# Optimization experiments

Measured on AMD Instinct MI355X. Metric: run time of the kernel, lower is better.

The kernel has to match this reference:

```python
import jax, jax.numpy as jnp
import numpy as np

B, S, D, H, E, K = 4, 2048, 1024, 2048, 8, 2
MU, GAMMA, LN_EPS = 0.7, 1.0, 1e-5


def setup_inputs() -> dict:
    key = jax.random.key(0)
    ks = jax.random.split(key, 8)
    inv_d = 1.0 / np.sqrt(D)
    inv_h = 1.0 / np.sqrt(H)
    return {
        "x": jax.random.normal(ks[0], (B, S, D), dtype=jnp.float32),
        "momentum": jax.random.normal(ks[1], (B, S, D), dtype=jnp.float32),
        "Wg": jax.random.normal(ks[2], (D, E), dtype=jnp.float32) * inv_d,
        "bg": jnp.zeros((E,), dtype=jnp.float32),
        "W1": jax.random.normal(ks[3], (E, D, H), dtype=jnp.float32) * inv_d,
        "b1": jnp.zeros((E, H), dtype=jnp.float32),
        "W2": jax.random.normal(ks[4], (E, H, D), dtype=jnp.float32) * inv_h,
        "b2": jnp.zeros((E, D), dtype=jnp.float32),
        "ln_g": jnp.ones((D,), dtype=jnp.float32),
        "ln_b": jnp.zeros((D,), dtype=jnp.float32),
    }


def reference(x, momentum, Wg, bg, W1, b1, W2, b2, ln_g, ln_b):
    # --- TopKGate: linear router, softmax over top-k logits, zeros elsewhere ---
    logits = jnp.einsum("bsd,de->bse", x, Wg) + bg            # [B,S,E]
    top_v, top_i = jax.lax.top_k(logits, K)                    # [B,S,K]
    top_w = jax.nn.softmax(top_v, axis=-1)                     # [B,S,K]
    gates = jnp.sum(jax.nn.one_hot(top_i, E, dtype=x.dtype) * top_w[..., None], axis=-2)  # [B,S,E]

    # --- Dense all-expert FFN (faithful to the original per-expert loop) ---
    h = jax.nn.relu(jnp.einsum("bsd,edh->bseh", x, W1) + b1)   # [B,S,E,H]
    eo = jnp.einsum("bseh,ehd->bsed", h, W2) + b2              # [B,S,E,D]
    expert_outputs = jnp.einsum("bse,bsed->bsd", gates, eo)    # [B,S,D]

    # --- Momentum update + residual + LayerNorm ---
    new_momentum = -expert_outputs + MU * momentum
    out = x + GAMMA * new_momentum
    mean = jnp.mean(out, axis=-1, keepdims=True)
    var = jnp.mean(jnp.square(out - mean), axis=-1, keepdims=True)
    out = (out - mean) * jax.lax.rsqrt(var + LN_EPS) * ln_g + ln_b
    return out, new_momentum
```

## Files before the change

### kernel.cpp

```cpp
#include <hip/hip_runtime.h>

#define TT 8192
#define DD 1024
#define HHH 2048
#define EE 8
#define MUf 0.7f
#define GAMMAf 1.0f
#define LNEPS 1e-5f

typedef __bf16 bf16x8 __attribute__((ext_vector_type(8)));
typedef float floatx4 __attribute__((ext_vector_type(4)));

__device__ __forceinline__ unsigned short f2bf(float f) {
  unsigned u = __float_as_uint(f);
  u += 0x7FFFu + ((u >> 16) & 1u);
  return (unsigned short)(u >> 16);
}
__device__ __forceinline__ float bf2f(unsigned short u) {
  return __uint_as_float(((unsigned)u) << 16);
}
__device__ __forceinline__ void load_lds16(const void* g, void* l) {
  __builtin_amdgcn_global_load_lds(
      (__attribute__((address_space(1))) void*)g,
      (__attribute__((address_space(3))) void*)l,
      16, 0, 0);
}

__global__ __launch_bounds__(256) void cvt_router_kernel(
    const float* __restrict__ x, const float* __restrict__ Wg, const float* __restrict__ bg,
    unsigned short* __restrict__ xb,
    int* __restrict__ pair_e, float* __restrict__ pair_w) {
  int tid = threadIdx.x;
  size_t gi = (size_t)blockIdx.x * 2048 + (size_t)tid * 8;
  const float4* s = (const float4*)(x + gi);
  float4 a = s[0], b = s[1];
  unsigned r0 = f2bf(a.x) | ((unsigned)f2bf(a.y) << 16);
  unsigned r1 = f2bf(a.z) | ((unsigned)f2bf(a.w) << 16);
  unsigned r2 = f2bf(b.x) | ((unsigned)f2bf(b.y) << 16);
  unsigned r3 = f2bf(b.z) | ((unsigned)f2bf(b.w) << 16);
  ((uint4*)xb)[blockIdx.x * 256 + tid] = make_uint4(r0, r1, r2, r3);

  float xa[8] = {a.x, a.y, a.z, a.w, b.x, b.y, b.z, b.w};
  int d0 = (tid & 127) * 8;
  const float* wbase = Wg + (size_t)d0 * EE;
  float acc[EE];
#pragma unroll
  for (int e = 0; e < EE; ++e) acc[e] = 0.f;
#pragma unroll
  for (int i = 0; i < 8; ++i) {
    float4 w0 = *(const float4*)(wbase + i * EE);
    float4 w1 = *(const float4*)(wbase + i * EE + 4);
    acc[0] += xa[i] * w0.x; acc[1] += xa[i] * w0.y;
    acc[2] += xa[i] * w0.z; acc[3] += xa[i] * w0.w;
    acc[4] += xa[i] * w1.x; acc[5] += xa[i] * w1.y;
    acc[6] += xa[i] * w1.z; acc[7] += xa[i] * w1.w;
  }
#pragma unroll
  for (int e = 0; e < EE; ++e) {
#pragma unroll
    for (int off = 32; off > 0; off >>= 1) acc[e] += __shfl_xor(acc[e], off);
  }
  __shared__ float rs[4][EE];
  int wv = tid >> 6;
  if ((tid & 63) == 0) {
#pragma unroll
    for (int e = 0; e < EE; ++e) rs[wv][e] = acc[e];
  }
  __syncthreads();
  if ((tid & 127) == 0) {
    int half = tid >> 7;
    int t = blockIdx.x * 2 + half;
    float v[EE];
#pragma unroll
    for (int e = 0; e < EE; ++e) v[e] = rs[2 * half][e] + rs[2 * half + 1][e] + bg[e];
    int i0 = 0;
#pragma unroll
    for (int e = 1; e < EE; ++e) if (v[e] > v[i0]) i0 = e;
    int i1 = (i0 == 0) ? 1 : 0;
#pragma unroll
    for (int e = 0; e < EE; ++e) if (e != i0 && v[e] > v[i1]) i1 = e;
    float w1e = __expf(v[i1] - v[i0]);
    float inv = 1.f / (1.f + w1e);
    pair_e[2 * t] = i0;     pair_w[2 * t] = inv;
    pair_e[2 * t + 1] = i1; pair_w[2 * t + 1] = w1e * inv;
  }
}

__global__ __launch_bounds__(256) void count_kernel(const int* __restrict__ pair_e,
                                                    int* __restrict__ counts) {
  __shared__ int lh[EE];
  int tid = threadIdx.x;
  if (tid < EE) lh[tid] = 0;
  __syncthreads();
  int p = blockIdx.x * 256 + tid;
  atomicAdd(&lh[pair_e[p]], 1);
  __syncthreads();
  if (tid < EE) atomicAdd(&counts[tid], lh[tid]);
}

__global__ void prefix_kernel(const int* __restrict__ counts, int* __restrict__ offs,
                              int* __restrict__ cursor) {
  if (threadIdx.x == 0) {
    int s = 0;
    for (int e = 0; e < EE; ++e) { offs[e] = s; cursor[e] = s; s += counts[e]; }
    offs[EE] = s;
  }
}

__global__ __launch_bounds__(256) void scatter_kernel(const int* __restrict__ pair_e,
                                                      int* __restrict__ cursor,
                                                      int* __restrict__ pair_rows) {
  __shared__ int lh[EE];
  __shared__ int lb[EE];
  int tid = threadIdx.x;
  if (tid < EE) lh[tid] = 0;
  __syncthreads();
  int p = blockIdx.x * 256 + tid;
  int e = pair_e[p];
  int r = atomicAdd(&lh[e], 1);
  __syncthreads();
  if (tid < EE) lb[tid] = atomicAdd(&cursor[tid], lh[tid]);
  __syncthreads();
  pair_rows[lb[e] + r] = p;
}

__global__ __launch_bounds__(256) void transpose_cvt_kernel(const float* __restrict__ in,
                                                            unsigned short* __restrict__ out,
                                                            int R, int C) {
  __shared__ float tile[32][33];
  int e = blockIdx.z;
  const float* src = in + (size_t)e * R * C;
  unsigned short* dst = out + (size_t)e * R * C;
  int c0 = blockIdx.x * 32, r0 = blockIdx.y * 32;
  int tx = threadIdx.x, ty = threadIdx.y;
#pragma unroll
  for (int i = 0; i < 32; i += 8)
    tile[ty + i][tx] = src[(size_t)(r0 + ty + i) * C + (c0 + tx)];
  __syncthreads();
#pragma unroll
  for (int i = 0; i < 32; i += 8)
    dst[(size_t)(c0 + ty + i) * R + (r0 + tx)] = f2bf(tile[tx][ty + i]);
}

template <int MODE>
__global__ __launch_bounds__(256, 3) void moe_gemm_kernel(
    const unsigned short* __restrict__ Amat, const unsigned short* __restrict__ Bmat,
    const float* __restrict__ bias, const int* __restrict__ offsets,
    const int* __restrict__ pair_rows, const float* __restrict__ pair_w,
    unsigned short* __restrict__ Out, int Kd, int Nd, int nxlog) {
  int d = blockIdx.x;
  int e = d & 7;
  int lin = d >> 3;
  int mt = lin >> nxlog;
  int n0 = (lin & ((1 << nxlog) - 1)) << 7;
  int off = offsets[e];
  int cnt = offsets[e + 1] - off;
  if (mt * 128 >= cnt) return;
  int tid = threadIdx.x;
  int lane = tid & 63, wid = tid >> 6;

  __shared__ unsigned short As[3][128 * 32];
  __shared__ unsigned short Bs[3][128 * 32];

  const unsigned short* Bex = Bmat + (size_t)e * Nd * Kd;

  int csw = (((tid & 3) ^ ((tid >> 2) & 3)) * 8);
  const unsigned short* aptr[2];
  const unsigned short* bptr[2];
#pragma unroll
  for (int P = 0; P < 2; ++P) {
    int row = P * 64 + (tid >> 2);
    int sa = mt * 128 + row;
    if (sa >= cnt) sa = cnt - 1;
    int gr = (MODE == 0) ? (pair_rows[off + sa] >> 1) : (off + sa);
    aptr[P] = Amat + (size_t)gr * Kd + csw;
    bptr[P] = Bex + (size_t)(n0 + row) * Kd + csw;
  }

  int wm = (wid >> 1) * 64, wn = (wid & 1) * 64;
  int lr = lane & 15;
  int t4 = lane >> 4;
  int lka = ((t4 ^ (lr & 3)) * 8);

  floatx4 acc[4][4];
#pragma unroll
  for (int m = 0; m < 4; ++m)
#pragma unroll
    for (int n = 0; n < 4; ++n) acc[m][n] = (floatx4){0.f, 0.f, 0.f, 0.f};

  int NT = Kd >> 5;
#pragma unroll
  for (int P = 0; P < 2; ++P) {
    load_lds16(aptr[P], &As[0][P * 2048] + tid * 8);
    load_lds16(bptr[P], &Bs[0][P * 2048] + tid * 8);
  }
#pragma unroll
  for (int P = 0; P < 2; ++P) {
    load_lds16(aptr[P] + 32, &As[1][P * 2048] + tid * 8);
    load_lds16(bptr[P] + 32, &Bs[1][P * 2048] + tid * 8);
  }

  for (int kt = 0; kt < NT; ++kt) {
    int pf = kt + 2;
    if (pf < NT) {
      int ko = pf * 32;
      int pb = pf - (pf / 3) * 3;
#pragma unroll
      for (int P = 0; P < 2; ++P) {
        load_lds16(aptr[P] + ko, &As[pb][P * 2048] + tid * 8);
        load_lds16(bptr[P] + ko, &Bs[pb][P * 2048] + tid * 8);
      }
    }
    asm volatile("s_waitcnt vmcnt(8)" ::: "memory");
    __builtin_amdgcn_s_barrier();
    int b = kt - (kt / 3) * 3;
    bf16x8 af[4], bfr[4];
#pragma unroll
    for (int m = 0; m < 4; ++m)
      af[m] = *(const bf16x8*)(&As[b][(wm + m * 16 + lr) * 32 + lka]);
#pragma unroll
    for (int n = 0; n < 4; ++n)
      bfr[n] = *(const bf16x8*)(&Bs[b][(wn + n * 16 + lr) * 32 + lka]);
#pragma unroll
    for (int m = 0; m < 4; ++m)
#pragma unroll
      for (int n = 0; n < 4; ++n)
        acc[m][n] = __builtin_amdgcn_mfma_f32_16x16x32_bf16(af[m], bfr[n], acc[m][n], 0, 0, 0);
    __builtin_amdgcn_sched_barrier(0);
    __builtin_amdgcn_s_barrier();
  }

  int rem = cnt - mt * 128;
  if (rem > 128) rem = 128;
#pragma unroll
  for (int m = 0; m < 4; ++m) {
#pragma unroll
    for (int j = 0; j < 4; ++j) {
      int lrr = wm + m * 16 + ((lane >> 4) << 2) + j;
      if (lrr < rem) {
        int s = mt * 128 + lrr;
        size_t orow;
        float scale = 1.f;
        if (MODE == 0) {
          orow = (size_t)(off + s) * Nd;
        } else {
          int p = pair_rows[off + s];
          orow = (size_t)p * Nd;
          scale = pair_w[p];
        }
#pragma unroll
        for (int n = 0; n < 4; ++n) {
          int col = n0 + wn + n * 16 + lr;
          float v = acc[m][n][j] + bias[e * Nd + col];
          if (MODE == 0) v = fmaxf(v, 0.f);
          else v *= scale;
          Out[orow + col] = f2bf(v);
        }
      }
    }
  }
}

__global__ __launch_bounds__(256) void final_kernel(
    const float* __restrict__ x, const float* __restrict__ mom,
    const unsigned short* __restrict__ pairout, const float* __restrict__ ln_g,
    const float* __restrict__ ln_b, float* __restrict__ outp, float* __restrict__ nmp) {
  int t = blockIdx.x, tid = threadIdx.x;
  int d0 = tid * 4;
  size_t rowoff = (size_t)t * DD;
  const unsigned short* p0 = pairout + (size_t)(2 * t) * DD;
  const unsigned short* p1 = p0 + DD;
  float4 xv = *(const float4*)(x + rowoff + d0);
  float4 mv = *(const float4*)(mom + rowoff + d0);
  ushort4 u0 = *(const ushort4*)(p0 + d0);
  ushort4 u1 = *(const ushort4*)(p1 + d0);
  float eo[4] = {bf2f(u0.x) + bf2f(u1.x), bf2f(u0.y) + bf2f(u1.y),
                 bf2f(u0.z) + bf2f(u1.z), bf2f(u0.w) + bf2f(u1.w)};
  float xa[4] = {xv.x, xv.y, xv.z, xv.w};
  float ma[4] = {mv.x, mv.y, mv.z, mv.w};
  float o[4], nm[4];
  float s1 = 0.f, s2 = 0.f;
#pragma unroll
  for (int j = 0; j < 4; ++j) {
    nm[j] = MUf * ma[j] - eo[j];
    o[j] = xa[j] + GAMMAf * nm[j];
    s1 += o[j];
    s2 += o[j] * o[j];
  }
  *(float4*)(nmp + rowoff + d0) = make_float4(nm[0], nm[1], nm[2], nm[3]);
#pragma unroll
  for (int off = 32; off > 0; off >>= 1) {
    s1 += __shfl_xor(s1, off);
    s2 += __shfl_xor(s2, off);
  }
  __shared__ float rs[8];
  int wid = tid >> 6, lane = tid & 63;
  if (lane == 0) { rs[wid] = s1; rs[4 + wid] = s2; }
  __syncthreads();
  s1 = rs[0] + rs[1] + rs[2] + rs[3];
  s2 = rs[4] + rs[5] + rs[6] + rs[7];
  float mean = s1 * (1.f / DD);
  float var = s2 * (1.f / DD) - mean * mean;
  float rstd = rsqrtf(var + LNEPS);
  float4 g = *(const float4*)(ln_g + d0);
  float4 bb = *(const float4*)(ln_b + d0);
  float ga[4] = {g.x, g.y, g.z, g.w}, ba[4] = {bb.x, bb.y, bb.z, bb.w};
  float res[4];
#pragma unroll
  for (int j = 0; j < 4; ++j) res[j] = (o[j] - mean) * rstd * ga[j] + ba[j];
  *(float4*)(outp + rowoff + d0) = make_float4(res[0], res[1], res[2], res[3]);
}

extern "C" void kernel_launch(void* const* d_in, const int* in_sizes, int n_in,
                              void* d_out, int out_size, void* d_ws, size_t ws_size,
                              hipStream_t stream) {
  const float* x   = (const float*)d_in[0];
  const float* mom = (const float*)d_in[1];
  const float* Wg  = (const float*)d_in[2];
  const float* bg  = (const float*)d_in[3];
  const float* W1  = (const float*)d_in[4];
  const float* b1  = (const float*)d_in[5];
  const float* W2  = (const float*)d_in[6];
  const float* b2  = (const float*)d_in[7];
  const float* lng = (const float*)d_in[8];
  const float* lnb = (const float*)d_in[9];
  (void)in_sizes; (void)n_in; (void)out_size; (void)ws_size;
  float* outp = (float*)d_out;
  float* nmp  = outp + (size_t)TT * DD;

  char* base = (char*)d_ws;
  size_t off = 0;
  auto carve = [&](size_t bytes) {
    void* p = base + off;
    off += (bytes + 255) & ~(size_t)255;
    return p;
  };
  unsigned short* xb   = (unsigned short*)carve((size_t)TT * DD * 2);
  unsigned short* w1t  = (unsigned short*)carve((size_t)EE * HHH * DD * 2);
  unsigned short* w2t  = (unsigned short*)carve((size_t)EE * DD * HHH * 2);
  unsigned short* hbuf = (unsigned short*)carve((size_t)2 * TT * HHH * 2);
  unsigned short* pout = (unsigned short*)carve((size_t)2 * TT * DD * 2);
  int*   pair_e    = (int*)carve((size_t)2 * TT * 4);
  float* pair_w    = (float*)carve((size_t)2 * TT * 4);
  int*   pair_rows = (int*)carve((size_t)2 * TT * 4);
  int*   counts    = (int*)carve(256);
  int*   offs      = (int*)carve(256);
  int*   cursor    = (int*)carve(256);

  hipMemsetAsync(counts, 0, EE * sizeof(int), stream);
  cvt_router_kernel<<<TT / 2, 256, 0, stream>>>(x, Wg, bg, xb, pair_e, pair_w);
  count_kernel<<<(2 * TT) / 256, 256, 0, stream>>>(pair_e, counts);
  prefix_kernel<<<1, 64, 0, stream>>>(counts, offs, cursor);
  scatter_kernel<<<(2 * TT) / 256, 256, 0, stream>>>(pair_e, cursor, pair_rows);
  transpose_cvt_kernel<<<dim3(HHH / 32, DD / 32, EE), dim3(32, 8, 1), 0, stream>>>(W1, w1t, DD, HHH);
  transpose_cvt_kernel<<<dim3(DD / 32, HHH / 32, EE), dim3(32, 8, 1), 0, stream>>>(W2, w2t, HHH, DD);
  moe_gemm_kernel<0><<<EE * (HHH / 128) * 128, 256, 0, stream>>>(
      xb, w1t, b1, offs, pair_rows, pair_w, hbuf, DD, HHH, 4);
  moe_gemm_kernel<1><<<EE * (DD / 128) * 128, 256, 0, stream>>>(
      hbuf, w2t, b2, offs, pair_rows, pair_w, pout, HHH, DD, 3);
  final_kernel<<<TT, 256, 0, stream>>>(x, mom, pout, lng, lnb, outp, nmp);
}
```

Baseline: 323.0 us.

## Vectorize weight transpose with 64x64 tiles and use single barrier per GEMM k-step

```diff
diff --git a/kernel.cpp b/kernel.cpp
--- a/kernel.cpp
+++ b/kernel.cpp
@@ -127,19 +127,32 @@
 __global__ __launch_bounds__(256) void transpose_cvt_kernel(const float* __restrict__ in,
                                                             unsigned short* __restrict__ out,
                                                             int R, int C) {
-  __shared__ float tile[32][33];
+  __shared__ float tile[64][65];
   int e = blockIdx.z;
   const float* src = in + (size_t)e * R * C;
   unsigned short* dst = out + (size_t)e * R * C;
-  int c0 = blockIdx.x * 32, r0 = blockIdx.y * 32;
-  int tx = threadIdx.x, ty = threadIdx.y;
-#pragma unroll
-  for (int i = 0; i < 32; i += 8)
-    tile[ty + i][tx] = src[(size_t)(r0 + ty + i) * C + (c0 + tx)];
-  __syncthreads();
-#pragma unroll
-  for (int i = 0; i < 32; i += 8)
-    dst[(size_t)(c0 + ty + i) * R + (r0 + tx)] = f2bf(tile[tx][ty + i]);
+  int c0 = blockIdx.x * 64, r0 = blockIdx.y * 64;
+  int t = threadIdx.x;
+  int q = t & 15, r = t >> 4;
+#pragma unroll
+  for (int i = 0; i < 4; ++i) {
+    int rr = r + 16 * i;
+    float4 v = *(const float4*)(src + (size_t)(r0 + rr) * C + c0 + q * 4);
+    tile[rr][q * 4 + 0] = v.x; tile[rr][q * 4 + 1] = v.y;
+    tile[rr][q * 4 + 2] = v.z; tile[rr][q * 4 + 3] = v.w;
+  }
+  __syncthreads();
+  int g = t & 15, cc = t >> 4;
+#pragma unroll
+  for (int i = 0; i < 4; ++i) {
+    int c = cc + 16 * i;
+    ushort4 o;
+    o.x = f2bf(tile[g * 4 + 0][c]);
+    o.y = f2bf(tile[g * 4 + 1][c]);
+    o.z = f2bf(tile[g * 4 + 2][c]);
+    o.w = f2bf(tile[g * 4 + 3][c]);
+    *(ushort4*)(dst + (size_t)(c0 + c) * R + r0 + g * 4) = o;
+  }
 }
 
 template <int MODE>
@@ -201,6 +214,13 @@
   }
 
   for (int kt = 0; kt < NT; ++kt) {
+    if (kt + 1 < NT) {
+      asm volatile("s_waitcnt vmcnt(4)" ::: "memory");
+    } else {
+      asm volatile("s_waitcnt vmcnt(0)" ::: "memory");
+    }
+    __builtin_amdgcn_s_barrier();
+    __builtin_amdgcn_sched_barrier(0);
     int pf = kt + 2;
     if (pf < NT) {
       int ko = pf * 32;
@@ -211,8 +231,6 @@
         load_lds16(bptr[P] + ko, &Bs[pb][P * 2048] + tid * 8);
       }
     }
-    asm volatile("s_waitcnt vmcnt(8)" ::: "memory");
-    __builtin_amdgcn_s_barrier();
     int b = kt - (kt / 3) * 3;
     bf16x8 af[4], bfr[4];
 #pragma unroll
@@ -226,8 +244,6 @@
 #pragma unroll
       for (int n = 0; n < 4; ++n)
         acc[m][n] = __builtin_amdgcn_mfma_f32_16x16x32_bf16(af[m], bfr[n], acc[m][n], 0, 0, 0);
-    __builtin_amdgcn_sched_barrier(0);
-    __builtin_amdgcn_s_barrier();
   }
 
   int rem = cnt - mt * 128;
@@ -352,8 +368,8 @@
   count_kernel<<<(2 * TT) / 256, 256, 0, stream>>>(pair_e, counts);
   prefix_kernel<<<1, 64, 0, stream>>>(counts, offs, cursor);
   scatter_kernel<<<(2 * TT) / 256, 256, 0, stream>>>(pair_e, cursor, pair_rows);
-  transpose_cvt_kernel<<<dim3(HHH / 32, DD / 32, EE), dim3(32, 8, 1), 0, stream>>>(W1, w1t, DD, HHH);
-  transpose_cvt_kernel<<<dim3(DD / 32, HHH / 32, EE), dim3(32, 8, 1), 0, stream>>>(W2, w2t, HHH, DD);
+  transpose_cvt_kernel<<<dim3(HHH / 64, DD / 64, EE), 256, 0, stream>>>(W1, w1t, DD, HHH);
+  transpose_cvt_kernel<<<dim3(DD / 64, HHH / 64, EE), 256, 0, stream>>>(W2, w2t, HHH, DD);
   moe_gemm_kernel<0><<<EE * (HHH / 128) * 128, 256, 0, stream>>>(
       xb, w1t, b1, offs, pair_rows, pair_w, hbuf, DD, HHH, 4);
   moe_gemm_kernel<1><<<EE * (DD / 128) * 128, 256, 0, stream>>>(
```

New measurement: 320.6 us. About the same (-0.7%).
